# Performance work log

Hardware: AMD Instinct MI355X
Metric: run time of the kernel (lower is better)

Reference implementation:

```python
import jax, jax.numpy as jnp
import numpy as np

# Per-layer (in_dim, hidden) for the 6 stacked LSTM layers:
# rnn_inp: (1,64),(64,64),(64,64); rnn_out: (64,1),(1,1),(1,1)
_LAYER_DIMS = [(1, 64), (64, 64), (64, 64), (64, 1), (1, 1), (1, 1)]
_LAYER_NAMES = ['a0', 'a1', 'a2', 'b0', 'b1', 'b2']


def _lstm_layer(x, w_ih, w_hh, b_ih, b_hh):
    """Single unidirectional LSTM layer, PyTorch gate order (i, f, g, o).
    x: [B, T, Din]; w_ih: [4H, Din]; w_hh: [4H, H]; biases: [4H]. Returns [B, T, H]."""
    H = w_hh.shape[1]
    B = x.shape[0]
    # Input projection for all timesteps at once (one big GEMM).
    pre = jnp.einsum('btd,gd->btg', x, w_ih) + b_ih + b_hh  # [B, T, 4H]
    pre_t = jnp.swapaxes(pre, 0, 1)  # [T, B, 4H]

    def step(carry, xt):
        h, c = carry
        gates = xt + h @ w_hh.T  # [B, 4H]
        i, f, g, o = jnp.split(gates, 4, axis=-1)
        i = jax.nn.sigmoid(i)
        f = jax.nn.sigmoid(f)
        g = jnp.tanh(g)
        o = jax.nn.sigmoid(o)
        c = f * c + i * g
        h = o * jnp.tanh(c)
        return (h, c), h

    h0 = jnp.zeros((B, H), x.dtype)
    (_, _), hs = jax.lax.scan(step, (h0, h0), pre_t)  # hs: [T, B, H]
    return jnp.swapaxes(hs, 0, 1)


def setup_inputs() -> dict:
    key = jax.random.key(0)
    B, T = 256, 512
    inp = {}
    k, key = jax.random.split(key)
    inp['x'] = jax.random.normal(k, (B, T, 1), dtype=jnp.float32)
    for name, (din, h) in zip(_LAYER_NAMES, _LAYER_DIMS):
        s = 1.0 / np.sqrt(h)  # PyTorch LSTM init scale U(-1/sqrt(H), 1/sqrt(H))
        k1, k2, k3, k4, key = jax.random.split(key, 5)
        inp[f'w_ih_{name}'] = jax.random.uniform(k1, (4 * h, din), jnp.float32, -s, s)
        inp[f'w_hh_{name}'] = jax.random.uniform(k2, (4 * h, h), jnp.float32, -s, s)
        inp[f'b_ih_{name}'] = jax.random.uniform(k3, (4 * h,), jnp.float32, -s, s)
        inp[f'b_hh_{name}'] = jax.random.uniform(k4, (4 * h,), jnp.float32, -s, s)
    return inp


def reference(x,
              w_ih_a0, w_hh_a0, b_ih_a0, b_hh_a0,
              w_ih_a1, w_hh_a1, b_ih_a1, b_hh_a1,
              w_ih_a2, w_hh_a2, b_ih_a2, b_hh_a2,
              w_ih_b0, w_hh_b0, b_ih_b0, b_hh_b0,
              w_ih_b1, w_hh_b1, b_ih_b1, b_hh_b1,
              w_ih_b2, w_hh_b2, b_ih_b2, b_hh_b2):
    layers = [
        (w_ih_a0, w_hh_a0, b_ih_a0, b_hh_a0),
        (w_ih_a1, w_hh_a1, b_ih_a1, b_hh_a1),
        (w_ih_a2, w_hh_a2, b_ih_a2, b_hh_a2),
        (w_ih_b0, w_hh_b0, b_ih_b0, b_hh_b0),
        (w_ih_b1, w_hh_b1, b_ih_b1, b_hh_b1),
        (w_ih_b2, w_hh_b2, b_ih_b2, b_hh_b2),
    ]
    h = x
    for w_ih, w_hh, b_ih, b_hh in layers:
        h = _lstm_layer(h, w_ih, w_hh, b_ih, b_hh)
    # activation between the two LSTM stacks is identity (activation_type='identity')
    return h  # [B, T, 1]
```

## Files before the change

kernel.cpp:

```cpp
#include <hip/hip_runtime.h>


#define BB 256
#define TT 512
#define CH 4
#define NS 16
#define NW (TT / CH)
#define HP 72
#define PP 260

typedef _Float16 v2h __attribute__((ext_vector_type(2)));
typedef _Float16 v8h __attribute__((ext_vector_type(8)));
typedef float v4f __attribute__((ext_vector_type(4)));

__device__ __forceinline__ float sig_(float x) {
  return __builtin_amdgcn_rcpf(1.f + __builtin_amdgcn_exp2f(-1.44269504f * x));
}
__device__ __forceinline__ float tanh_(float x) {
  return __builtin_fmaf(2.f, __builtin_amdgcn_rcpf(1.f + __builtin_amdgcn_exp2f(-2.88539008f * x)), -1.f);
}

template <int K>
__device__ __forceinline__ float qb_(float v) {
  return __int_as_float(__builtin_amdgcn_update_dpp(
      0, __float_as_int(v), (K | (K << 2) | (K << 4) | (K << 6)), 0xF, 0xF, true));
}

#if __has_builtin(__builtin_amdgcn_fdot2)
#define FDOT2(acc, a, b) (acc) = __builtin_amdgcn_fdot2((a), (b), (acc), false)
#else
#define FDOT2(acc, a, b) \
  (acc) = __builtin_fmaf((float)(a)[0], (float)(b)[0], \
          __builtin_fmaf((float)(a)[1], (float)(b)[1], (acc)))
#endif
#define KEEPP(a) asm volatile("" : "+v"(a))
#define PIN16(w)                                                            \
  do {                                                                      \
    _Pragma("unroll") for (int _i = 0; _i < 16; ++_i) KEEPP((w)[_i]);       \
  } while (0)

#define WAITP(i, v)                                                           \
  while (__hip_atomic_load(&prog[i], __ATOMIC_ACQUIRE,                        \
                           __HIP_MEMORY_SCOPE_WORKGROUP) < (v)) {             \
    __builtin_amdgcn_s_sleep(1);                                              \
  }
#define POSTP(i, v)                                                           \
  do {                                                                        \
    asm volatile("s_waitcnt lgkmcnt(0)" ::: "memory");                        \
    if (lane == 0)                                                            \
      __hip_atomic_store(&prog[i], (v), __ATOMIC_RELEASE,                     \
                         __HIP_MEMORY_SCOPE_WORKGROUP);                       \
  } while (0)

__device__ __forceinline__ v2h bc2h_(int v) { return __builtin_bit_cast(v2h, v); }

__device__ __forceinline__ void load_h64(const _Float16* p, v2h hv[32]) {
  const int4* hp = reinterpret_cast<const int4*>(p);
#pragma unroll
  for (int i = 0; i < 8; ++i) {
    int4 blk = hp[i];
    hv[4 * i + 0] = bc2h_(blk.x);
    hv[4 * i + 1] = bc2h_(blk.y);
    hv[4 * i + 2] = bc2h_(blk.z);
    hv[4 * i + 3] = bc2h_(blk.w);
  }
}

__device__ __forceinline__ void load_row_pair(const float* src, v2h* lo, v2h* hi) {
  const float4* p = reinterpret_cast<const float4*>(src);
#pragma unroll
  for (int i = 0; i < 8; ++i) {
    float4 v = p[i];
    lo[2 * i]     = v2h{(_Float16)v.x, (_Float16)v.y};
    lo[2 * i + 1] = v2h{(_Float16)v.z, (_Float16)v.w};
  }
#pragma unroll
  for (int i = 0; i < 8; ++i) {
    float4 v = p[8 + i];
    hi[2 * i]     = v2h{(_Float16)v.x, (_Float16)v.y};
    hi[2 * i + 1] = v2h{(_Float16)v.z, (_Float16)v.w};
  }
}

__device__ __forceinline__ v8h ldbfrag_(const float* W, int t, int kc, int lane) {
  const int row = 16 * t + (lane & 15);
  const float* p = W + row * 64 + 32 * kc + 4 * (lane >> 4);
  float4 fa = *reinterpret_cast<const float4*>(p);
  float4 fb = *reinterpret_cast<const float4*>(p + 16);
  return v8h{(_Float16)fa.x, (_Float16)fa.y, (_Float16)fa.z, (_Float16)fa.w,
             (_Float16)fb.x, (_Float16)fb.y, (_Float16)fb.z, (_Float16)fb.w};
}

__device__ __forceinline__ void ldafrag_(const _Float16* hprev, int q4,
                                         v8h& A0, v8h& A1) {
  const char* hp = (const char*)hprev + 8 * q4;
  int2 r00 = *(const int2*)(hp);
  int2 r01 = *(const int2*)(hp + 32);
  int2 r10 = *(const int2*)(hp + 64);
  int2 r11 = *(const int2*)(hp + 96);
  A0 = __builtin_bit_cast(v8h, int4{r00.x, r00.y, r01.x, r01.y});
  A1 = __builtin_bit_cast(v8h, int4{r10.x, r10.y, r11.x, r11.y});
}

__device__ __forceinline__ void regafrag_(float hA, int lane, const int ba[8],
                                          v8h& A0, v8h& A1) {
  int hnb = __builtin_amdgcn_update_dpp(0, __float_as_int(hA), 0xB1, 0xF, 0xF, true);
  float hn = __int_as_float(hnb);
  float lo = (lane & 1) ? hn : hA;
  float hi = (lane & 1) ? hA : hn;
  int pkw = __builtin_bit_cast(int, v2h{(_Float16)lo, (_Float16)hi});
  int w0 = __builtin_amdgcn_ds_bpermute(ba[0], pkw);
  int w1 = __builtin_amdgcn_ds_bpermute(ba[1], pkw);
  int w2 = __builtin_amdgcn_ds_bpermute(ba[2], pkw);
  int w3 = __builtin_amdgcn_ds_bpermute(ba[3], pkw);
  int w4 = __builtin_amdgcn_ds_bpermute(ba[4], pkw);
  int w5 = __builtin_amdgcn_ds_bpermute(ba[5], pkw);
  int w6 = __builtin_amdgcn_ds_bpermute(ba[6], pkw);
  int w7 = __builtin_amdgcn_ds_bpermute(ba[7], pkw);
  A0 = __builtin_bit_cast(v8h, int4{w0, w1, w2, w3});
  A1 = __builtin_bit_cast(v8h, int4{w4, w5, w6, w7});
}

__device__ __forceinline__ void rec_mv_(const v8h bfr[16][2],
                                        const v8h& A0, const v8h& A1,
                                        bool s0, bool s1, float p[4]) {
  const v4f z = {0.f, 0.f, 0.f, 0.f};
  v4f acc[16];
#pragma unroll
  for (int tl = 0; tl < 16; ++tl) {
    v4f d = __builtin_amdgcn_mfma_f32_16x16x32_f16(A0, bfr[tl][0], z, 0, 0, 0);
    acc[tl] = __builtin_amdgcn_mfma_f32_16x16x32_f16(A1, bfr[tl][1], d, 0, 0, 0);
  }
#pragma unroll
  for (int g = 0; g < 4; ++g) {
    float v01 = s0 ? acc[4 * g + 1][0] : acc[4 * g + 0][0];
    float v23 = s0 ? acc[4 * g + 3][0] : acc[4 * g + 2][0];
    p[g] = s1 ? v23 : v01;
  }
}

__global__ __attribute__((amdgpu_flat_work_group_size(384, 384),
                          amdgpu_waves_per_eu(2, 2)))
void lstm_pipe_k(
    const float* __restrict__ x,
    const float* __restrict__ wih_a0, const float* __restrict__ whh_a0,
    const float* __restrict__ bih_a0, const float* __restrict__ bhh_a0,
    const float* __restrict__ wih_a1, const float* __restrict__ whh_a1,
    const float* __restrict__ bih_a1, const float* __restrict__ bhh_a1,
    const float* __restrict__ wih_a2, const float* __restrict__ whh_a2,
    const float* __restrict__ bih_a2, const float* __restrict__ bhh_a2,
    const float* __restrict__ wih_b0, const float* __restrict__ whh_b0,
    const float* __restrict__ bih_b0, const float* __restrict__ bhh_b0,
    const float* __restrict__ wih_b1, const float* __restrict__ whh_b1,
    const float* __restrict__ bih_b1, const float* __restrict__ bhh_b1,
    const float* __restrict__ wih_b2, const float* __restrict__ whh_b2,
    const float* __restrict__ bih_b2, const float* __restrict__ bhh_b2,
    float* __restrict__ out)
{
  const int b = blockIdx.x;
  const int tid = threadIdx.x;
  const int wave = tid >> 6;
  const int lane = tid & 63;

  __shared__ __align__(16) _Float16 hh[3][NS][HP];
  __shared__ __align__(16) float pj[2][NS][PP];
  __shared__ float xs[TT];
  __shared__ int prog[6];

  for (int i = tid; i < TT; i += 384) xs[i] = x[(size_t)b * TT + i];
  for (int i = tid; i < 3 * NS * HP / 2; i += 384) reinterpret_cast<int*>(hh)[i] = 0;
  if (tid < 6) prog[tid] = 0;

  union UW {
    v8h bfr[16][2];
    v2h wtb[2][16];
  } u;

  float bias[4] = {0.f, 0.f, 0.f, 0.f};
  float wi0_[4] = {0.f, 0.f, 0.f, 0.f};
  float whb0[4] = {}, wi1b[4] = {}, wh1b[4] = {}, bb1[4] = {},
        wi2b[4] = {}, wh2b[4] = {}, bb2[4] = {};

  if (wave == 0) {
#pragma unroll
    for (int t = 0; t < 16; ++t) {
      u.bfr[t][0] = ldbfrag_(whh_a0, t, 0, lane);
      u.bfr[t][1] = ldbfrag_(whh_a0, t, 1, lane);
    }
#pragma unroll
    for (int q = 0; q < 4; ++q) {
      const int row = q * 64 + lane;
      bias[q] = bih_a0[row] + bhh_a0[row];
      wi0_[q] = wih_a0[row];
    }
  } else if (wave == 1) {
#pragma unroll
    for (int t = 0; t < 16; ++t) {
      u.bfr[t][0] = ldbfrag_(whh_a1, t, 0, lane);
      u.bfr[t][1] = ldbfrag_(whh_a1, t, 1, lane);
    }
#pragma unroll
    for (int q = 0; q < 4; ++q) bias[q] = bih_a1[q * 64 + lane] + bhh_a1[q * 64 + lane];
  } else if (wave == 2) {
#pragma unroll
    for (int t = 0; t < 16; ++t) {
      u.bfr[t][0] = ldbfrag_(whh_a2, t, 0, lane);
      u.bfr[t][1] = ldbfrag_(whh_a2, t, 1, lane);
    }
#pragma unroll
    for (int q = 0; q < 4; ++q) bias[q] = bih_a2[q * 64 + lane] + bhh_a2[q * 64 + lane];
  } else if (wave == 3) {
    const int q = lane & 3;
    load_row_pair(wih_b0 + q * 64, u.wtb[0], u.wtb[1]);
    bias[0] = bih_b0[q] + bhh_b0[q];
#pragma unroll
    for (int k = 0; k < 4; ++k) {
      whb0[k] = whh_b0[k];
      wi1b[k] = wih_b1[k]; wh1b[k] = whh_b1[k]; bb1[k] = bih_b1[k] + bhh_b1[k];
      wi2b[k] = wih_b2[k]; wh2b[k] = whh_b2[k]; bb2[k] = bih_b2[k] + bhh_b2[k];
    }
    PIN16(u.wtb[0]); PIN16(u.wtb[1]);
  } else if (wave == 4) {
#pragma unroll
    for (int t = 0; t < 16; ++t) {
      u.bfr[t][0] = ldbfrag_(wih_a1, t, 0, lane);
      u.bfr[t][1] = ldbfrag_(wih_a1, t, 1, lane);
    }
  } else {
#pragma unroll
    for (int t = 0; t < 16; ++t) {
      u.bfr[t][0] = ldbfrag_(wih_a2, t, 0, lane);
      u.bfr[t][1] = ldbfrag_(wih_a2, t, 1, lane);
    }
  }
  __syncthreads();

  float c = 0.f;
  float h0b = 0.f, c0b = 0.f, h1b = 0.f, c1b = 0.f, h2b = 0.f, c2b = 0.f;
  const int q4 = lane >> 4;
  const bool s0 = q4 & 1, s1 = q4 & 2;
  const v4f z = {0.f, 0.f, 0.f, 0.f};

  int ba[8];
#pragma unroll
  for (int cc = 0; cc < 4; ++cc) {
#pragma unroll
    for (int w = 0; w < 2; ++w) ba[cc * 2 + w] = 4 * (16 * cc + 4 * q4 + 2 * w);
  }

  if (wave == 0) {
    __builtin_amdgcn_s_setprio(1);
    float hA = 0.f;
    for (int k = 0; k < NW; ++k) {
      if (k >= 4) { WAITP(4, k - 3); }
      const int t0 = k * CH;
      for (int s = 0; s < CH; ++s) {
        const int t = t0 + s;
        v8h A0, A1;
        regafrag_(hA, lane, ba, A0, A1);
        if (s > 0) hh[0][(t - 1) & (NS - 1)][lane] = (_Float16)hA;
        float p[4];
        rec_mv_(u.bfr, A0, A1, s0, s1, p);
        const float xv = xs[t];
        float p0 = __builtin_fmaf(wi0_[0], xv, p[0] + bias[0]);
        float p1 = __builtin_fmaf(wi0_[1], xv, p[1] + bias[1]);
        float p2 = __builtin_fmaf(wi0_[2], xv, p[2] + bias[2]);
        float p3 = __builtin_fmaf(wi0_[3], xv, p[3] + bias[3]);
        float gi = sig_(p0), gf = sig_(p1), gg = tanh_(p2), go = sig_(p3);
        c = __builtin_fmaf(gf, c, gi * gg);
        hA = go * tanh_(c);
      }
      hh[0][(t0 + CH - 1) & (NS - 1)][lane] = (_Float16)hA;
      POSTP(0, k + 1);
    }
    __builtin_amdgcn_s_setprio(0);
  } else if (wave == 1) {
    __builtin_amdgcn_s_setprio(1);
    float hA = 0.f;
    for (int k = 0; k < NW; ++k) {
      WAITP(4, k + 1);
      if (k >= 4) { WAITP(5, k - 3); }
      const int t0 = k * CH;
      for (int s = 0; s < CH; ++s) {
        const int t = t0 + s;
        v8h A0, A1;
        regafrag_(hA, lane, ba, A0, A1);
        if (s > 0) hh[1][(t - 1) & (NS - 1)][lane] = (_Float16)hA;
        float4 pr = *reinterpret_cast<const float4*>(&pj[0][t & (NS - 1)][lane * 4]);
        float p[4];
        rec_mv_(u.bfr, A0, A1, s0, s1, p);
        float p0 = p[0] + bias[0] + pr.x;
        float p1 = p[1] + bias[1] + pr.y;
        float p2 = p[2] + bias[2] + pr.z;
        float p3 = p[3] + bias[3] + pr.w;
        float gi = sig_(p0), gf = sig_(p1), gg = tanh_(p2), go = sig_(p3);
        c = __builtin_fmaf(gf, c, gi * gg);
        hA = go * tanh_(c);
      }
      hh[1][(t0 + CH - 1) & (NS - 1)][lane] = (_Float16)hA;
      POSTP(1, k + 1);
    }
    __builtin_amdgcn_s_setprio(0);
  } else if (wave == 2) {
    __builtin_amdgcn_s_setprio(1);
    float hA = 0.f;
    for (int k = 0; k < NW; ++k) {
      WAITP(5, k + 1);
      if (k >= 4) { WAITP(3, k - 3); }
      const int t0 = k * CH;
      for (int s = 0; s < CH; ++s) {
        const int t = t0 + s;
        v8h A0, A1;
        regafrag_(hA, lane, ba, A0, A1);
        if (s > 0) hh[2][(t - 1) & (NS - 1)][lane] = (_Float16)hA;
        float4 pr = *reinterpret_cast<const float4*>(&pj[1][t & (NS - 1)][lane * 4]);
        float p[4];
        rec_mv_(u.bfr, A0, A1, s0, s1, p);
        float p0 = p[0] + bias[0] + pr.x;
        float p1 = p[1] + bias[1] + pr.y;
        float p2 = p[2] + bias[2] + pr.z;
        float p3 = p[3] + bias[3] + pr.w;
        float gi = sig_(p0), gf = sig_(p1), gg = tanh_(p2), go = sig_(p3);
        c = __builtin_fmaf(gf, c, gi * gg);
        hA = go * tanh_(c);
      }
      hh[2][(t0 + CH - 1) & (NS - 1)][lane] = (_Float16)hA;
      POSTP(2, k + 1);
    }
    __builtin_amdgcn_s_setprio(0);
  } else if (wave == 3) {
    for (int k = 0; k < NW; ++k) {
      WAITP(2, k + 1);
      const int t0 = k * CH;
      for (int s = 0; s < CH; ++s) {
        const int t = t0 + s;
        v2h hv[32];
        load_h64(&hh[2][t & (NS - 1)][0], hv);
        float pga = bias[0], pgb = 0.f;
#pragma unroll
        for (int j = 0; j < 16; ++j) {
          FDOT2(pga, u.wtb[0][j], hv[j]);
          FDOT2(pgb, u.wtb[1][j], hv[16 + j]);
        }
        float pg = pga + pgb;
        float p_i = qb_<0>(pg), p_f = qb_<1>(pg), p_g = qb_<2>(pg), p_o = qb_<3>(pg);
        float i0 = sig_(__builtin_fmaf(whb0[0], h0b, p_i));
        float f0 = sig_(__builtin_fmaf(whb0[1], h0b, p_f));
        float g0 = tanh_(__builtin_fmaf(whb0[2], h0b, p_g));
        float o0 = sig_(__builtin_fmaf(whb0[3], h0b, p_o));
        c0b = __builtin_fmaf(f0, c0b, i0 * g0);
        h0b = o0 * tanh_(c0b);
        float i1 = sig_(bb1[0] + __builtin_fmaf(wi1b[0], h0b, wh1b[0] * h1b));
        float f1 = sig_(bb1[1] + __builtin_fmaf(wi1b[1], h0b, wh1b[1] * h1b));
        float g1 = tanh_(bb1[2] + __builtin_fmaf(wi1b[2], h0b, wh1b[2] * h1b));
        float o1 = sig_(bb1[3] + __builtin_fmaf(wi1b[3], h0b, wh1b[3] * h1b));
        c1b = __builtin_fmaf(f1, c1b, i1 * g1);
        h1b = o1 * tanh_(c1b);
        float i2 = sig_(bb2[0] + __builtin_fmaf(wi2b[0], h1b, wh2b[0] * h2b));
        float f2 = sig_(bb2[1] + __builtin_fmaf(wi2b[1], h1b, wh2b[1] * h2b));
        float g2 = tanh_(bb2[2] + __builtin_fmaf(wi2b[2], h1b, wh2b[2] * h2b));
        float o2 = sig_(bb2[3] + __builtin_fmaf(wi2b[3], h1b, wh2b[3] * h2b));
        c2b = __builtin_fmaf(f2, c2b, i2 * g2);
        h2b = o2 * tanh_(c2b);
        if (lane == 0) out[(size_t)b * TT + t] = h2b;
      }
      POSTP(3, k + 1);
    }
  } else if (wave == 4) {
    for (int k = 0; k < NW; ++k) {
      WAITP(0, k + 1);
      if (k >= 4) { WAITP(1, k - 3); }
      const int t0 = k * CH;
      const int slotb = (t0 + (lane & 15)) & (NS - 1);
      v8h Bf0, Bf1;
      ldafrag_(&hh[0][slotb][0], q4, Bf0, Bf1);
      float* pbase = &pj[0][slotb][0] + 16 * q4;
      const bool wr = (lane & 15) < CH;
#pragma unroll
      for (int tl = 0; tl < 16; ++tl) {
        v4f acc = __builtin_amdgcn_mfma_f32_16x16x32_f16(u.bfr[tl][0], Bf0, z, 0, 0, 0);
        acc = __builtin_amdgcn_mfma_f32_16x16x32_f16(u.bfr[tl][1], Bf1, acc, 0, 0, 0);
        if (wr) {
          const int o = 64 * (tl & 3) + (tl >> 2);
          pbase[o] = acc[0]; pbase[o + 4] = acc[1];
          pbase[o + 8] = acc[2]; pbase[o + 12] = acc[3];
        }
        __builtin_amdgcn_sched_barrier(0);
      }
      POSTP(4, k + 1);
    }
  } else {
    for (int k = 0; k < NW; ++k) {
      WAITP(1, k + 1);
      if (k >= 4) { WAITP(2, k - 3); }
      const int t0 = k * CH;
      const int slotb = (t0 + (lane & 15)) & (NS - 1);
      v8h Bf0, Bf1;
      ldafrag_(&hh[1][slotb][0], q4, Bf0, Bf1);
      float* pbase = &pj[1][slotb][0] + 16 * q4;
      const bool wr = (lane & 15) < CH;
#pragma unroll
      for (int tl = 0; tl < 16; ++tl) {
        v4f acc = __builtin_amdgcn_mfma_f32_16x16x32_f16(u.bfr[tl][0], Bf0, z, 0, 0, 0);
        acc = __builtin_amdgcn_mfma_f32_16x16x32_f16(u.bfr[tl][1], Bf1, acc, 0, 0, 0);
        if (wr) {
          const int o = 64 * (tl & 3) + (tl >> 2);
          pbase[o] = acc[0]; pbase[o + 4] = acc[1];
          pbase[o + 8] = acc[2]; pbase[o + 12] = acc[3];
        }
        __builtin_amdgcn_sched_barrier(0);
      }
      POSTP(5, k + 1);
    }
  }
}

extern "C" void kernel_launch(void* const* d_in, const int* in_sizes, int n_in,
                              void* d_out, int out_size, void* d_ws, size_t ws_size,
                              hipStream_t stream) {
  const float* x      = (const float*)d_in[0];
  const float* wih_a0 = (const float*)d_in[1];
  const float* whh_a0 = (const float*)d_in[2];
  const float* bih_a0 = (const float*)d_in[3];
  const float* bhh_a0 = (const float*)d_in[4];
  const float* wih_a1 = (const float*)d_in[5];
  const float* whh_a1 = (const float*)d_in[6];
  const float* bih_a1 = (const float*)d_in[7];
  const float* bhh_a1 = (const float*)d_in[8];
  const float* wih_a2 = (const float*)d_in[9];
  const float* whh_a2 = (const float*)d_in[10];
  const float* bih_a2 = (const float*)d_in[11];
  const float* bhh_a2 = (const float*)d_in[12];
  const float* wih_b0 = (const float*)d_in[13];
  const float* whh_b0 = (const float*)d_in[14];
  const float* bih_b0 = (const float*)d_in[15];
  const float* bhh_b0 = (const float*)d_in[16];
  const float* wih_b1 = (const float*)d_in[17];
  const float* whh_b1 = (const float*)d_in[18];
  const float* bih_b1 = (const float*)d_in[19];
  const float* bhh_b1 = (const float*)d_in[20];
  const float* wih_b2 = (const float*)d_in[21];
  const float* whh_b2 = (const float*)d_in[22];
  const float* bih_b2 = (const float*)d_in[23];
  const float* bhh_b2 = (const float*)d_in[24];
  float* out = (float*)d_out;

  lstm_pipe_k<<<BB, 384, 0, stream>>>(
      x,
      wih_a0, whh_a0, bih_a0, bhh_a0,
      wih_a1, whh_a1, bih_a1, bhh_a1,
      wih_a2, whh_a2, bih_a2, bhh_a2,
      wih_b0, whh_b0, bih_b0, bhh_b0,
      wih_b1, whh_b1, bih_b1, bhh_b1,
      wih_b2, whh_b2, bih_b2, bhh_b2,
      out);
}
```

Before: 347.9 us.

## Use LDS round-trip for recurrent h fragments and respread waves across SIMDs

Replaces the DPP plus ds_bpermute register shuffle that built the MFMA A-fragment of the previous hidden state with a store of h to shared memory each step followed by ldafrag_ loads. Launches 512 threads, with two idle waves that return right after setup, so the projection waves move to indices 6 and 7, which likely changes how waves map to SIMDs. The projected-input float4 is now prefetched one step ahead. This trades bpermute latency on the serial recurrence for an extra LDS write-then-read per step, and it relies on in-wave LDS ordering.

After: 336.8 us. -3.2%, faster.

```diff
diff --git a/kernel.cpp b/kernel.cpp
--- a/kernel.cpp
+++ b/kernel.cpp
@@ -102,25 +102,6 @@
   A1 = __builtin_bit_cast(v8h, int4{r10.x, r10.y, r11.x, r11.y});
 }
 
-__device__ __forceinline__ void regafrag_(float hA, int lane, const int ba[8],
-                                          v8h& A0, v8h& A1) {
-  int hnb = __builtin_amdgcn_update_dpp(0, __float_as_int(hA), 0xB1, 0xF, 0xF, true);
-  float hn = __int_as_float(hnb);
-  float lo = (lane & 1) ? hn : hA;
-  float hi = (lane & 1) ? hA : hn;
-  int pkw = __builtin_bit_cast(int, v2h{(_Float16)lo, (_Float16)hi});
-  int w0 = __builtin_amdgcn_ds_bpermute(ba[0], pkw);
-  int w1 = __builtin_amdgcn_ds_bpermute(ba[1], pkw);
-  int w2 = __builtin_amdgcn_ds_bpermute(ba[2], pkw);
-  int w3 = __builtin_amdgcn_ds_bpermute(ba[3], pkw);
-  int w4 = __builtin_amdgcn_ds_bpermute(ba[4], pkw);
-  int w5 = __builtin_amdgcn_ds_bpermute(ba[5], pkw);
-  int w6 = __builtin_amdgcn_ds_bpermute(ba[6], pkw);
-  int w7 = __builtin_amdgcn_ds_bpermute(ba[7], pkw);
-  A0 = __builtin_bit_cast(v8h, int4{w0, w1, w2, w3});
-  A1 = __builtin_bit_cast(v8h, int4{w4, w5, w6, w7});
-}
-
 __device__ __forceinline__ void rec_mv_(const v8h bfr[16][2],
                                         const v8h& A0, const v8h& A1,
                                         bool s0, bool s1, float p[4]) {
@@ -139,7 +120,7 @@
   }
 }
 
-__global__ __attribute__((amdgpu_flat_work_group_size(384, 384),
+__global__ __attribute__((amdgpu_flat_work_group_size(512, 512),
                           amdgpu_waves_per_eu(2, 2)))
 void lstm_pipe_k(
     const float* __restrict__ x,
@@ -165,11 +146,11 @@
   __shared__ __align__(16) _Float16 hh[3][NS][HP];
   __shared__ __align__(16) float pj[2][NS][PP];
   __shared__ float xs[TT];
-  __shared__ int prog[6];
-
-  for (int i = tid; i < TT; i += 384) xs[i] = x[(size_t)b * TT + i];
-  for (int i = tid; i < 3 * NS * HP / 2; i += 384) reinterpret_cast<int*>(hh)[i] = 0;
-  if (tid < 6) prog[tid] = 0;
+  __shared__ int prog[8];
+
+  for (int i = tid; i < TT; i += 512) xs[i] = x[(size_t)b * TT + i];
+  for (int i = tid; i < 3 * NS * HP / 2; i += 512) reinterpret_cast<int*>(hh)[i] = 0;
+  if (tid < 8) prog[tid] = 0;
 
   union UW {
     v8h bfr[16][2];
@@ -220,20 +201,21 @@
       wi2b[k] = wih_b2[k]; wh2b[k] = whh_b2[k]; bb2[k] = bih_b2[k] + bhh_b2[k];
     }
     PIN16(u.wtb[0]); PIN16(u.wtb[1]);
-  } else if (wave == 4) {
+  } else if (wave == 6) {
+#pragma unroll
+    for (int t = 0; t < 16; ++t) {
+      u.bfr[t][0] = ldbfrag_(wih_a2, t, 0, lane);
+      u.bfr[t][1] = ldbfrag_(wih_a2, t, 1, lane);
+    }
+  } else if (wave == 7) {
 #pragma unroll
     for (int t = 0; t < 16; ++t) {
       u.bfr[t][0] = ldbfrag_(wih_a1, t, 0, lane);
       u.bfr[t][1] = ldbfrag_(wih_a1, t, 1, lane);
     }
-  } else {
-#pragma unroll
-    for (int t = 0; t < 16; ++t) {
-      u.bfr[t][0] = ldbfrag_(wih_a2, t, 0, lane);
-      u.bfr[t][1] = ldbfrag_(wih_a2, t, 1, lane);
-    }
   }
   __syncthreads();
+  if (wave == 4 || wave == 5) return;
 
   float c = 0.f;
   float h0b = 0.f, c0b = 0.f, h1b = 0.f, c1b = 0.f, h2b = 0.f, c2b = 0.f;
@@ -241,24 +223,15 @@
   const bool s0 = q4 & 1, s1 = q4 & 2;
   const v4f z = {0.f, 0.f, 0.f, 0.f};
 
-  int ba[8];
-#pragma unroll
-  for (int cc = 0; cc < 4; ++cc) {
-#pragma unroll
-    for (int w = 0; w < 2; ++w) ba[cc * 2 + w] = 4 * (16 * cc + 4 * q4 + 2 * w);
-  }
-
   if (wave == 0) {
     __builtin_amdgcn_s_setprio(1);
-    float hA = 0.f;
-    for (int k = 0; k < NW; ++k) {
-      if (k >= 4) { WAITP(4, k - 3); }
+    for (int k = 0; k < NW; ++k) {
+      if (k >= 4) { WAITP(7, k - 3); }
       const int t0 = k * CH;
       for (int s = 0; s < CH; ++s) {
         const int t = t0 + s;
         v8h A0, A1;
-        regafrag_(hA, lane, ba, A0, A1);
-        if (s > 0) hh[0][(t - 1) & (NS - 1)][lane] = (_Float16)hA;
+        ldafrag_(&hh[0][(t + NS - 1) & (NS - 1)][0], q4, A0, A1);
         float p[4];
         rec_mv_(u.bfr, A0, A1, s0, s1, p);
         const float xv = xs[t];
@@ -268,25 +241,25 @@
         float p3 = __builtin_fmaf(wi0_[3], xv, p[3] + bias[3]);
         float gi = sig_(p0), gf = sig_(p1), gg = tanh_(p2), go = sig_(p3);
         c = __builtin_fmaf(gf, c, gi * gg);
-        hA = go * tanh_(c);
-      }
-      hh[0][(t0 + CH - 1) & (NS - 1)][lane] = (_Float16)hA;
+        hh[0][t & (NS - 1)][lane] = (_Float16)(go * tanh_(c));
+      }
       POSTP(0, k + 1);
     }
     __builtin_amdgcn_s_setprio(0);
   } else if (wave == 1) {
     __builtin_amdgcn_s_setprio(1);
-    float hA = 0.f;
-    for (int k = 0; k < NW; ++k) {
-      WAITP(4, k + 1);
-      if (k >= 4) { WAITP(5, k - 3); }
-      const int t0 = k * CH;
+    for (int k = 0; k < NW; ++k) {
+      WAITP(7, k + 1);
+      if (k >= 4) { WAITP(6, k - 3); }
+      const int t0 = k * CH;
+      float4 pr = *reinterpret_cast<const float4*>(&pj[0][t0 & (NS - 1)][lane * 4]);
       for (int s = 0; s < CH; ++s) {
         const int t = t0 + s;
         v8h A0, A1;
-        regafrag_(hA, lane, ba, A0, A1);
-        if (s > 0) hh[1][(t - 1) & (NS - 1)][lane] = (_Float16)hA;
-        float4 pr = *reinterpret_cast<const float4*>(&pj[0][t & (NS - 1)][lane * 4]);
+        ldafrag_(&hh[1][(t + NS - 1) & (NS - 1)][0], q4, A0, A1);
+        float4 prn = pr;
+        if (s + 1 < CH)
+          prn = *reinterpret_cast<const float4*>(&pj[0][(t + 1) & (NS - 1)][lane * 4]);
         float p[4];
         rec_mv_(u.bfr, A0, A1, s0, s1, p);
         float p0 = p[0] + bias[0] + pr.x;
@@ -295,25 +268,26 @@
         float p3 = p[3] + bias[3] + pr.w;
         float gi = sig_(p0), gf = sig_(p1), gg = tanh_(p2), go = sig_(p3);
         c = __builtin_fmaf(gf, c, gi * gg);
-        hA = go * tanh_(c);
-      }
-      hh[1][(t0 + CH - 1) & (NS - 1)][lane] = (_Float16)hA;
+        hh[1][t & (NS - 1)][lane] = (_Float16)(go * tanh_(c));
+        pr = prn;
+      }
       POSTP(1, k + 1);
     }
     __builtin_amdgcn_s_setprio(0);
   } else if (wave == 2) {
     __builtin_amdgcn_s_setprio(1);
-    float hA = 0.f;
-    for (int k = 0; k < NW; ++k) {
-      WAITP(5, k + 1);
+    for (int k = 0; k < NW; ++k) {
+      WAITP(6, k + 1);
       if (k >= 4) { WAITP(3, k - 3); }
       const int t0 = k * CH;
+      float4 pr = *reinterpret_cast<const float4*>(&pj[1][t0 & (NS - 1)][lane * 4]);
       for (int s = 0; s < CH; ++s) {
         const int t = t0 + s;
         v8h A0, A1;
-        regafrag_(hA, lane, ba, A0, A1);
-        if (s > 0) hh[2][(t - 1) & (NS - 1)][lane] = (_Float16)hA;
-        float4 pr = *reinterpret_cast<const float4*>(&pj[1][t & (NS - 1)][lane * 4]);
+        ldafrag_(&hh[2][(t + NS - 1) & (NS - 1)][0], q4, A0, A1);
+        float4 prn = pr;
+        if (s + 1 < CH)
+          prn = *reinterpret_cast<const float4*>(&pj[1][(t + 1) & (NS - 1)][lane * 4]);
         float p[4];
         rec_mv_(u.bfr, A0, A1, s0, s1, p);
         float p0 = p[0] + bias[0] + pr.x;
@@ -322,9 +296,9 @@
         float p3 = p[3] + bias[3] + pr.w;
         float gi = sig_(p0), gf = sig_(p1), gg = tanh_(p2), go = sig_(p3);
         c = __builtin_fmaf(gf, c, gi * gg);
-        hA = go * tanh_(c);
-      }
-      hh[2][(t0 + CH - 1) & (NS - 1)][lane] = (_Float16)hA;
+        hh[2][t & (NS - 1)][lane] = (_Float16)(go * tanh_(c));
+        pr = prn;
+      }
       POSTP(2, k + 1);
     }
     __builtin_amdgcn_s_setprio(0);
@@ -366,7 +340,7 @@
       }
       POSTP(3, k + 1);
     }
-  } else if (wave == 4) {
+  } else if (wave == 7) {
     for (int k = 0; k < NW; ++k) {
       WAITP(0, k + 1);
       if (k >= 4) { WAITP(1, k - 3); }
@@ -387,7 +361,7 @@
         }
         __builtin_amdgcn_sched_barrier(0);
       }
-      POSTP(4, k + 1);
+      POSTP(7, k + 1);
     }
   } else {
     for (int k = 0; k < NW; ++k) {
@@ -410,7 +384,7 @@
         }
         __builtin_amdgcn_sched_barrier(0);
       }
-      POSTP(5, k + 1);
+      POSTP(6, k + 1);
     }
   }
 }
@@ -445,7 +419,7 @@
   const float* bhh_b2 = (const float*)d_in[24];
   float* out = (float*)d_out;
 
-  lstm_pipe_k<<<BB, 384, 0, stream>>>(
+  lstm_pipe_k<<<BB, 512, 0, stream>>>(
       x,
       wih_a0, whh_a0, bih_a0, bhh_a0,
       wih_a1, whh_a1, bih_a1, bhh_a1,
```
